# Kernel optimization log

Hardware: AMD Instinct MI355X
Metric: run time of the kernel (lower is better)

## Reference

```python
import jax, jax.numpy as jnp
import numpy as np

N = 100000
EPS = 1e-5


def sage_conv(x, edge_index, w_l, b_l, w_r):
    # PyG SAGEConv (aggr='mean'): out = lin_l(mean_{j in N(i)} x_j) + lin_r(x_i)
    src = edge_index[0]
    tgt = edge_index[1]
    msg = x[src]                                        # [E, d] gather
    agg = jax.ops.segment_sum(msg, tgt, num_segments=N)  # [N, d] scatter-add
    cnt = jax.ops.segment_sum(jnp.ones_like(tgt, dtype=x.dtype), tgt, num_segments=N)
    mean = agg / jnp.maximum(cnt, 1.0)[:, None]
    return mean @ w_l.T + b_l + x @ w_r.T


def batchnorm(h, gamma, beta):
    mu = jnp.mean(h, axis=0)
    var = jnp.var(h, axis=0)  # biased, matches torch BN training normalization
    return (h - mu) * jax.lax.rsqrt(var + EPS) * gamma + beta


def setup_inputs() -> dict:
    key = jax.random.key(0)
    ks = jax.random.split(key, 16)
    d_in, d_h, h1, h2 = 32, 64, 128, 64
    E = 1600000
    inp = {
        "x": jax.random.normal(ks[0], (N, d_in), dtype=jnp.float32),
        "edge_index": jax.random.randint(ks[1], (2, E), 0, N, dtype=jnp.int64),
        # SAGEConv 1 (bias in lin_l only)
        "w_l1": jax.random.normal(ks[2], (d_h, d_in), dtype=jnp.float32) * 0.1,
        "b_l1": jnp.zeros((d_h,), dtype=jnp.float32),
        "w_r1": jax.random.normal(ks[3], (d_h, d_in), dtype=jnp.float32) * 0.1,
        # SAGEConv 2
        "w_l2": jax.random.normal(ks[4], (d_h, d_h), dtype=jnp.float32) * 0.1,
        "b_l2": jnp.zeros((d_h,), dtype=jnp.float32),
        "w_r2": jax.random.normal(ks[5], (d_h, d_h), dtype=jnp.float32) * 0.1,
        # MLP head
        "fc1_w": jax.random.normal(ks[6], (h1, d_h), dtype=jnp.float32) * 0.1,
        "fc1_b": jnp.zeros((h1,), dtype=jnp.float32),
        "bn1_g": jnp.ones((h1,), dtype=jnp.float32),
        "bn1_b": jnp.zeros((h1,), dtype=jnp.float32),
        "fc2_w": jax.random.normal(ks[7], (h2, h1), dtype=jnp.float32) * 0.1,
        "fc2_b": jnp.zeros((h2,), dtype=jnp.float32),
        "bn2_g": jnp.ones((h2,), dtype=jnp.float32),
        "bn2_b": jnp.zeros((h2,), dtype=jnp.float32),
        "fc3_w": jax.random.normal(ks[8], (1, h2), dtype=jnp.float32) * 0.1,
        "fc3_b": jnp.zeros((1,), dtype=jnp.float32),
    }
    return inp


def reference(x, edge_index, w_l1, b_l1, w_r1, w_l2, b_l2, w_r2,
              fc1_w, fc1_b, bn1_g, bn1_b, fc2_w, fc2_b, bn2_g, bn2_b,
              fc3_w, fc3_b):
    h1 = jax.nn.relu(sage_conv(x, edge_index, w_l1, b_l1, w_r1))   # [N, 64]
    h2 = jax.nn.relu(sage_conv(h1, edge_index, w_l2, b_l2, w_r2))  # [N, 64]
    z = jax.nn.relu(batchnorm(h2 @ fc1_w.T + fc1_b, bn1_g, bn1_b))
    z = jax.nn.relu(batchnorm(z @ fc2_w.T + fc2_b, bn2_g, bn2_b))
    out = (z @ fc3_w.T + fc3_b).squeeze(-1)                        # [N]
    return (out, h1, h2)
```

## Files before the change

kernel.cpp:

```cpp
#include <hip/hip_runtime.h>

#define NN 100000
#define EPS 1e-5f

static const size_t OFF_ROWST  = 0;
static const size_t OFF_ROWEN  = 100000;
static const size_t OFF_ADJ    = 200000;
static const size_t OFF_AGG1   = 2886976;
static const size_t OFF_AGG2   = 6086976;
static const size_t OFF_PAIRS  = 2886976;
static const size_t OFF_XB     = 12486976;
static const size_t OFF_Z1     = 0;
static const size_t OFF_H1B    = 14086976;
static const size_t OFF_Z2     = 14086976;
static const size_t OFF_WSPL   = 20487000;
static const size_t OFF_BUKCNT = 20515712;
static const size_t OFF_STATS1 = 20515968;
static const size_t OFF_STATS2 = 20548736;
static const size_t OFF_COEF1  = 20565120;
static const size_t OFF_COEF2  = 20565376;
static const size_t OFF_BHIST  = 20565504;
static const size_t ZERO_START = 20515968;
static const size_t ZERO_INTS  = 49152;

#define NSLOT 128

#define WL1_HI 0
#define WL1_LO 2048
#define WR1_HI 4096
#define WR1_LO 6144
#define WL2_HI 8192
#define WL2_LO 12288
#define WR2_HI 16384
#define WR2_LO 20480
#define F1_HI  24576
#define F1_LO  32768
#define F2_HI  40960
#define F2_LO  49152

#define NBUK 256
#define BSHIFT 9
#define BCAP 10496
#define CHUNK 2048

typedef __attribute__((ext_vector_type(8))) short short8;
typedef __attribute__((ext_vector_type(4))) float f32x4;

#define MFMA_16x16x32(a, b, c) __builtin_amdgcn_mfma_f32_16x16x32_bf16(a, b, c, 0, 0, 0)

__device__ inline unsigned short f2bf(float f) {
  unsigned u = __builtin_bit_cast(unsigned, f);
  unsigned r = (u + 0x7fffu + ((u >> 16) & 1u)) >> 16;
  return (unsigned short)r;
}
__device__ inline float bf2f(unsigned short h) {
  unsigned u = ((unsigned)h) << 16;
  return __builtin_bit_cast(float, u);
}

template<bool BNIN>
__device__ inline void load_split(const float* __restrict__ p,
                                  const float* __restrict__ ca,
                                  const float* __restrict__ cc,
                                  short8& hi, short8& lo) {
  #pragma unroll
  for (int j = 0; j < 8; ++j) {
    float v = p[j];
    if (BNIN) v = fmaxf(v * ca[j] + cc[j], 0.f);
    unsigned short h = f2bf(v);
    hi[j] = (short)h;
    lo[j] = (short)f2bf(v - bf2f(h));
  }
}

struct WsplitArgs {
  const float* src[6];
  unsigned short* dhi[6];
  unsigned short* dlo[6];
  int n[6];
};
__global__ __launch_bounds__(256) void wsplit_k(WsplitArgs a) {
  int m = blockIdx.y;
  int n = a.n[m];
  for (int i = blockIdx.x * 256 + threadIdx.x; i < n; i += gridDim.x * 256) {
    float v = a.src[m][i];
    unsigned short h = f2bf(v);
    a.dhi[m][i] = h;
    a.dlo[m][i] = f2bf(v - bf2f(h));
  }
}

__global__ __launch_bounds__(256) void cvt_bf_k(const float* __restrict__ in,
                                                unsigned short* __restrict__ out,
                                                int n8) {
  int t = blockIdx.x * 256 + threadIdx.x;
  if (t >= n8) return;
  const float4* p = (const float4*)(in + (size_t)t * 8);
  float4 a = p[0], b = p[1];
  ushort4 u0, u1;
  u0.x = f2bf(a.x); u0.y = f2bf(a.y); u0.z = f2bf(a.z); u0.w = f2bf(a.w);
  u1.x = f2bf(b.x); u1.y = f2bf(b.y); u1.z = f2bf(b.z); u1.w = f2bf(b.w);
  ((ushort4*)(out + (size_t)t * 8))[0] = u0;
  ((ushort4*)(out + (size_t)t * 8))[1] = u1;
}

__global__ __launch_bounds__(256) void hista_k(const int* __restrict__ ei, int E,
                                               int* __restrict__ blockhist) {
  __shared__ int h[NBUK];
  int tid = threadIdx.x;
  h[tid] = 0;
  __syncthreads();
  int lo = blockIdx.x * CHUNK, hi = min(lo + CHUNK, E);
  for (int e = lo + tid; e < hi; e += 256) {
    int t = ei[E + e];
    if ((unsigned)t < NN) atomicAdd(&h[t >> BSHIFT], 1);
  }
  __syncthreads();
  blockhist[(size_t)blockIdx.x * NBUK + tid] = h[tid];
}

__global__ __launch_bounds__(256) void scanb_k(int* __restrict__ blockhist, int nch,
                                               int* __restrict__ bukcnt) {
  __shared__ int sh[256];
  int b = blockIdx.x, t = threadIdx.x;
  int run = 0;
  for (int base = 0; base < nch; base += 256) {
    int c = base + t;
    int v = (c < nch) ? blockhist[(size_t)c * NBUK + b] : 0;
    sh[t] = v;
    __syncthreads();
    for (int o = 1; o < 256; o <<= 1) {
      int u = (t >= o) ? sh[t - o] : 0;
      __syncthreads();
      sh[t] += u;
      __syncthreads();
    }
    if (c < nch) blockhist[(size_t)c * NBUK + b] = run + sh[t] - v;
    int tot = sh[255];
    __syncthreads();
    run += tot;
  }
  if (t == 0) bukcnt[b] = run;
}

__global__ __launch_bounds__(256) void scat_k(const int* __restrict__ ei, int E,
                                              const int* __restrict__ blockhist,
                                              unsigned* __restrict__ pairs) {
  __shared__ int wb[NBUK], cur[NBUK];
  int tid = threadIdx.x;
  wb[tid] = blockhist[(size_t)blockIdx.x * NBUK + tid];
  cur[tid] = 0;
  __syncthreads();
  int lo = blockIdx.x * CHUNK, hi = min(lo + CHUNK, E);
  for (int e = lo + tid; e < hi; e += 256) {
    int s = ei[e], t = ei[E + e];
    if ((unsigned)t >= NN) continue;
    if ((unsigned)s >= NN) s = 0;
    int b = t >> BSHIFT;
    int off = atomicAdd(&cur[b], 1);
    pairs[(size_t)b * BCAP + wb[b] + off] = ((unsigned)s << 9) | (unsigned)(t & 511);
  }
}

__global__ __launch_bounds__(256) void bfill2_k(const unsigned* __restrict__ pairs,
                                                const int* __restrict__ bukcnt,
                                                int* __restrict__ rowstart,
                                                int* __restrict__ rowend,
                                                int* __restrict__ adj) {
  __shared__ int d[512];
  __shared__ int part[256];
  int b = blockIdx.x;
  int t = threadIdx.x;
  int base = b * BCAP, cnt = bukcnt[b];
  d[t] = 0; d[t + 256] = 0;
  __syncthreads();
  for (int p = base + t; p < base + cnt; p += 256)
    atomicAdd(&d[pairs[p] & 511], 1);
  __syncthreads();
  int d0 = d[2 * t], d1 = d[2 * t + 1];
  part[t] = d0 + d1;
  __syncthreads();
  for (int o = 1; o < 256; o <<= 1) {
    int u = (t >= o) ? part[t - o] : 0;
    __syncthreads();
    part[t] += u;
    __syncthreads();
  }
  int e0 = (t > 0) ? part[t - 1] : 0;
  int e1 = e0 + d0;
  d[2 * t] = e0;
  d[2 * t + 1] = e1;
  int n0 = (b << BSHIFT) + 2 * t;
  if (n0 < NN)     { rowstart[n0]     = base + e0; rowend[n0]     = base + e1; }
  if (n0 + 1 < NN) { rowstart[n0 + 1] = base + e1; rowend[n0 + 1] = base + e1 + d1; }
  __syncthreads();
  for (int p = base + t; p < base + cnt; p += 256) {
    unsigned pr = pairs[p];
    int pos = atomicAdd(&d[pr & 511], 1);
    adj[base + pos] = (int)(pr >> 9);
  }
}

template<int K>
__global__ __launch_bounds__(256) void aggregate_bf(const unsigned short* __restrict__ xb,
                                                    const int* __restrict__ rowstart,
                                                    const int* __restrict__ rowend,
                                                    const int* __restrict__ adj,
                                                    float* __restrict__ agg) {
  constexpr int GL = K / 4;
  constexpr int NPB = 256 / GL;
  int lg = threadIdx.x & (GL - 1);
  int node = blockIdx.x * NPB + (threadIdx.x / GL);
  if (node >= NN) return;
  int s0 = rowstart[node], s1 = rowend[node];
  float4 a0 = {0,0,0,0}, a1 = {0,0,0,0}, a2 = {0,0,0,0}, a3 = {0,0,0,0};
  int e = s0;
  for (; e + 3 < s1; e += 4) {
    int i0 = adj[e], i1 = adj[e+1], i2 = adj[e+2], i3 = adj[e+3];
    ushort4 u0 = *(const ushort4*)(xb + (size_t)i0 * K + lg * 4);
    ushort4 u1 = *(const ushort4*)(xb + (size_t)i1 * K + lg * 4);
    ushort4 u2 = *(const ushort4*)(xb + (size_t)i2 * K + lg * 4);
    ushort4 u3 = *(const ushort4*)(xb + (size_t)i3 * K + lg * 4);
    a0.x += bf2f(u0.x); a0.y += bf2f(u0.y); a0.z += bf2f(u0.z); a0.w += bf2f(u0.w);
    a1.x += bf2f(u1.x); a1.y += bf2f(u1.y); a1.z += bf2f(u1.z); a1.w += bf2f(u1.w);
    a2.x += bf2f(u2.x); a2.y += bf2f(u2.y); a2.z += bf2f(u2.z); a2.w += bf2f(u2.w);
    a3.x += bf2f(u3.x); a3.y += bf2f(u3.y); a3.z += bf2f(u3.z); a3.w += bf2f(u3.w);
  }
  for (; e < s1; ++e) {
    ushort4 u = *(const ushort4*)(xb + (size_t)adj[e] * K + lg * 4);
    a0.x += bf2f(u.x); a0.y += bf2f(u.y); a0.z += bf2f(u.z); a0.w += bf2f(u.w);
  }
  float inv = 1.0f / fmaxf((float)(s1 - s0), 1.0f);
  float4 r;
  r.x = (a0.x + a1.x + a2.x + a3.x) * inv;
  r.y = (a0.y + a1.y + a2.y + a3.y) * inv;
  r.z = (a0.z + a1.z + a2.z + a3.z) * inv;
  r.w = (a0.w + a1.w + a2.w + a3.w) * inv;
  *(float4*)(agg + (size_t)node * K + lg * 4) = r;
}

template<int K, int C, bool SAGE, bool BNIN, bool RELU, bool BFOUT, bool STATS>
__global__ __launch_bounds__(256) void mfma_dense(const float* __restrict__ inA,
                                                  const float* __restrict__ inB,
                                                  const unsigned short* __restrict__ whiA,
                                                  const unsigned short* __restrict__ wloA,
                                                  const unsigned short* __restrict__ whiB,
                                                  const unsigned short* __restrict__ wloB,
                                                  const float* __restrict__ bias,
                                                  const float* __restrict__ coef,
                                                  float* __restrict__ out,
                                                  unsigned short* __restrict__ outb,
                                                  float* __restrict__ stats) {
  constexpr int KF = K / 32;
  constexpr int KC = K / 8;
  constexpr int SWZ = (KC < 8 ? KC : 8) - 1;
  __shared__ unsigned short swhiA[C * K], swloA[C * K];
  __shared__ unsigned short swhiB[SAGE ? C * K : 8], swloB[SAGE ? C * K : 8];
  __shared__ float ls[STATS ? C : 1], lq[STATS ? C : 1];

  int tid = threadIdx.x;
  for (int i = tid; i < C * KC; i += 256) {
    int col = i / KC, c = i % KC;
    int pos = col * KC + (c ^ (col & SWZ));
    ((short8*)swhiA)[pos] = ((const short8*)whiA)[i];
    ((short8*)swloA)[pos] = ((const short8*)wloA)[i];
    if (SAGE) {
      ((short8*)swhiB)[pos] = ((const short8*)whiB)[i];
      ((short8*)swloB)[pos] = ((const short8*)wloB)[i];
    }
  }
  if (STATS) {
    for (int i = tid; i < C; i += 256) { ls[i] = 0.f; lq[i] = 0.f; }
  }
  __syncthreads();

  int wid  = tid >> 6;
  int lane = tid & 63;
  int row0 = blockIdx.x * 64 + wid * 16;
  int r = lane & 15, g = lane >> 4;
  int arow = row0 + r; if (arow > NN - 1) arow = NN - 1;
  int koff = g * 8;

  short8 ahi[KF], alo[KF];
  short8 a2hi[SAGE ? KF : 1], a2lo[SAGE ? KF : 1];
  #pragma unroll
  for (int kf = 0; kf < KF; ++kf) {
    const float* p = inA + (size_t)arow * K + kf * 32 + koff;
    load_split<BNIN>(p, coef + kf * 32 + koff, coef + K + kf * 32 + koff,
                     ahi[kf], alo[kf]);
  }
  if (SAGE) {
    #pragma unroll
    for (int kf = 0; kf < KF; ++kf) {
      const float* p = inB + (size_t)arow * K + kf * 32 + koff;
      load_split<false>(p, nullptr, nullptr, a2hi[kf], a2lo[kf]);
    }
  }

  #pragma unroll
  for (int cf = 0; cf < C / 16; ++cf) {
    int col = cf * 16 + r;
    float bv = bias[col];
    f32x4 acc = {bv, bv, bv, bv};
    #pragma unroll
    for (int kf = 0; kf < KF; ++kf) {
      int c = kf * 4 + g;
      int pos = col * KC + (c ^ (col & SWZ));
      short8 whi = ((const short8*)swhiA)[pos];
      short8 wlo = ((const short8*)swloA)[pos];
      acc = MFMA_16x16x32(ahi[kf], whi, acc);
      acc = MFMA_16x16x32(ahi[kf], wlo, acc);
      acc = MFMA_16x16x32(alo[kf], whi, acc);
      if (SAGE) {
        short8 vhi = ((const short8*)swhiB)[pos];
        short8 vlo = ((const short8*)swloB)[pos];
        acc = MFMA_16x16x32(a2hi[kf], vhi, acc);
        acc = MFMA_16x16x32(a2hi[kf], vlo, acc);
        acc = MFMA_16x16x32(a2lo[kf], vhi, acc);
      }
    }
    if (STATS) {
      float s = 0.f, q = 0.f;
      #pragma unroll
      for (int j = 0; j < 4; ++j) {
        if (row0 + g * 4 + j < NN) {
          float v = acc[j];
          s += v; q += v * v;
        }
      }
      s += __shfl_xor(s, 16, 64); s += __shfl_xor(s, 32, 64);
      q += __shfl_xor(q, 16, 64); q += __shfl_xor(q, 32, 64);
      if (g == 0) { atomicAdd(&ls[col], s); atomicAdd(&lq[col], q); }
    }
    #pragma unroll
    for (int j = 0; j < 4; ++j) {
      int orow = row0 + g * 4 + j;
      if (orow < NN) {
        float v = acc[j];
        if (RELU) v = fmaxf(v, 0.f);
        out[(size_t)orow * C + col] = v;
        if (BFOUT) outb[(size_t)orow * C + col] = f2bf(v);
      }
    }
  }
  if (STATS) {
    __syncthreads();
    float* sl = stats + (size_t)(blockIdx.x & (NSLOT - 1)) * 2 * C;
    for (int i = tid; i < C; i += 256) {
      atomicAdd(&sl[i], ls[i]);
      atomicAdd(&sl[C + i], lq[i]);
    }
  }
}

__global__ void bncoef(const float* __restrict__ stats, const float* __restrict__ g,
                       const float* __restrict__ b, float* __restrict__ coef, int C) {
  int j = threadIdx.x;
  if (j >= C) return;
  float s = 0.f, q = 0.f;
  for (int sl = 0; sl < NSLOT; ++sl) {
    s += stats[(size_t)sl * 2 * C + j];
    q += stats[(size_t)sl * 2 * C + C + j];
  }
  float mu  = s * (1.0f / NN);
  float var = q * (1.0f / NN) - mu * mu;
  float a = g[j] * rsqrtf(var + EPS);
  coef[j] = a;
  coef[C + j] = b[j] - mu * a;
}

__global__ __launch_bounds__(256) void final_k(const float* __restrict__ z2,
                                               const float* __restrict__ coef,
                                               const float* __restrict__ fc3w,
                                               const float* __restrict__ fc3b,
                                               float* __restrict__ out) {
  int t = blockIdx.x * 256 + threadIdx.x;
  int i = t >> 6;
  int j = t & 63;
  if (i >= NN) return;
  float v = z2[(size_t)i * 64 + j];
  float p = fmaxf(v * coef[j] + coef[64 + j], 0.f) * fc3w[j];
  #pragma unroll
  for (int o = 32; o > 0; o >>= 1) p += __shfl_xor(p, o, 64);
  if (j == 0) out[i] = p + fc3b[0];
}

extern "C" void kernel_launch(void* const* d_in, const int* in_sizes, int n_in,
                              void* d_out, int out_size, void* d_ws, size_t ws_size,
                              hipStream_t stream) {
  const float* x     = (const float*)d_in[0];
  const int*   ei    = (const int*)d_in[1];
  const float* w_l1  = (const float*)d_in[2];
  const float* b_l1  = (const float*)d_in[3];
  const float* w_r1  = (const float*)d_in[4];
  const float* w_l2  = (const float*)d_in[5];
  const float* b_l2  = (const float*)d_in[6];
  const float* w_r2  = (const float*)d_in[7];
  const float* fc1_w = (const float*)d_in[8];
  const float* fc1_b = (const float*)d_in[9];
  const float* bn1_g = (const float*)d_in[10];
  const float* bn1_b = (const float*)d_in[11];
  const float* fc2_w = (const float*)d_in[12];
  const float* fc2_b = (const float*)d_in[13];
  const float* bn2_g = (const float*)d_in[14];
  const float* bn2_b = (const float*)d_in[15];
  const float* fc3_w = (const float*)d_in[16];
  const float* fc3_b = (const float*)d_in[17];

  const int E = in_sizes[1] / 2;

  float* ws       = (float*)d_ws;
  int*   rowstart = (int*)(ws + OFF_ROWST);
  int*   rowend   = (int*)(ws + OFF_ROWEN);
  int*   adj      = (int*)(ws + OFF_ADJ);
  float* agg1     = ws + OFF_AGG1;
  float* agg2     = ws + OFF_AGG2;
  unsigned short* xb  = (unsigned short*)(ws + OFF_XB);
  unsigned short* h1b = (unsigned short*)(ws + OFF_H1B);
  float* z1       = ws + OFF_Z1;
  float* z2       = ws + OFF_Z2;
  int*   bukcnt   = (int*)(ws + OFF_BUKCNT);
  float* stats1   = ws + OFF_STATS1;
  float* stats2   = ws + OFF_STATS2;
  float* coef1    = ws + OFF_COEF1;
  float* coef2    = ws + OFF_COEF2;
  unsigned* pairs = (unsigned*)(ws + OFF_PAIRS);
  int*   bhist    = (int*)(ws + OFF_BHIST);
  unsigned short* wspl = (unsigned short*)(ws + OFF_WSPL);

  float* outv = (float*)d_out;
  float* h1   = outv + NN;
  float* h2   = h1 + (size_t)NN * 64;

  hipMemsetAsync(ws + ZERO_START, 0, ZERO_INTS * sizeof(float), stream);

  WsplitArgs wa;
  wa.src[0] = w_l1;  wa.dhi[0] = wspl + WL1_HI; wa.dlo[0] = wspl + WL1_LO; wa.n[0] = 64 * 32;
  wa.src[1] = w_r1;  wa.dhi[1] = wspl + WR1_HI; wa.dlo[1] = wspl + WR1_LO; wa.n[1] = 64 * 32;
  wa.src[2] = w_l2;  wa.dhi[2] = wspl + WL2_HI; wa.dlo[2] = wspl + WL2_LO; wa.n[2] = 64 * 64;
  wa.src[3] = w_r2;  wa.dhi[3] = wspl + WR2_HI; wa.dlo[3] = wspl + WR2_LO; wa.n[3] = 64 * 64;
  wa.src[4] = fc1_w; wa.dhi[4] = wspl + F1_HI;  wa.dlo[4] = wspl + F1_LO;  wa.n[4] = 128 * 64;
  wa.src[5] = fc2_w; wa.dhi[5] = wspl + F2_HI;  wa.dlo[5] = wspl + F2_LO;  wa.n[5] = 64 * 128;
  wsplit_k<<<dim3(8, 6), 256, 0, stream>>>(wa);

  cvt_bf_k<<<(NN * 32 / 8 + 255) / 256, 256, 0, stream>>>(x, xb, NN * 32 / 8);

  const int NCH = (E + CHUNK - 1) / CHUNK;
  hista_k<<<NCH, 256, 0, stream>>>(ei, E, bhist);
  scanb_k<<<NBUK, 256, 0, stream>>>(bhist, NCH, bukcnt);
  scat_k<<<NCH, 256, 0, stream>>>(ei, E, bhist, pairs);
  bfill2_k<<<NBUK, 256, 0, stream>>>(pairs, bukcnt, rowstart, rowend, adj);

  const int MB = (NN + 63) / 64;

  aggregate_bf<32><<<(NN + 31) / 32, 256, 0, stream>>>(xb, rowstart, rowend, adj, agg1);
  mfma_dense<32, 64, true, false, true, true, false><<<MB, 256, 0, stream>>>(
      agg1, x, wspl + WL1_HI, wspl + WL1_LO, wspl + WR1_HI, wspl + WR1_LO,
      b_l1, nullptr, h1, h1b, nullptr);

  aggregate_bf<64><<<(NN + 15) / 16, 256, 0, stream>>>(h1b, rowstart, rowend, adj, agg2);
  mfma_dense<64, 64, true, false, true, false, false><<<MB, 256, 0, stream>>>(
      agg2, h1, wspl + WL2_HI, wspl + WL2_LO, wspl + WR2_HI, wspl + WR2_LO,
      b_l2, nullptr, h2, nullptr, nullptr);

  mfma_dense<64, 128, false, false, false, false, true><<<MB, 256, 0, stream>>>(
      h2, nullptr, wspl + F1_HI, wspl + F1_LO, nullptr, nullptr,
      fc1_b, nullptr, z1, nullptr, stats1);
  bncoef<<<1, 128, 0, stream>>>(stats1, bn1_g, bn1_b, coef1, 128);

  mfma_dense<128, 64, false, true, false, false, true><<<MB, 256, 0, stream>>>(
      z1, nullptr, wspl + F2_HI, wspl + F2_LO, nullptr, nullptr,
      fc2_b, coef1, z2, nullptr, stats2);
  bncoef<<<1, 64, 0, stream>>>(stats2, bn2_g, bn2_b, coef2, 64);

  final_k<<<(NN * 64 + 255) / 256, 256, 0, stream>>>(z2, coef2, fc3_w, fc3_b, outv);
}
```

Baseline: 241.9 us.

## Store MLP intermediates z1/z2 in bf16 and process two row tiles per block

The fc1 and fc2 pre-activations (z1, z2) are now written only as bf16 rather than fp32. fc2's input loader and the final kernel read them back as bf16, which roughly halves the bandwidth spent on these intermediates. Separately, each dense-kernel block now loops over two 64-row tiles, halving the grid and amortizing the shared-memory weight load per block. The cost is lost precision in z1/z2: BN stats are still taken from the fp32 accumulators, but normalization is then applied to bf16-rounded values.

After: 250.3 us. 1.03x slower.

```diff
diff --git a/kernel.cpp b/kernel.cpp
--- a/kernel.cpp
+++ b/kernel.cpp
@@ -10,9 +10,9 @@
 static const size_t OFF_AGG2   = 6086976;
 static const size_t OFF_PAIRS  = 2886976;
 static const size_t OFF_XB     = 12486976;
-static const size_t OFF_Z1     = 0;
+static const size_t OFF_Z1B    = 0;
 static const size_t OFF_H1B    = 14086976;
-static const size_t OFF_Z2     = 14086976;
+static const size_t OFF_Z2B    = 14086976;
 static const size_t OFF_WSPL   = 20487000;
 static const size_t OFF_BUKCNT = 20515712;
 static const size_t OFF_STATS1 = 20515968;
@@ -58,14 +58,14 @@
   return __builtin_bit_cast(float, u);
 }
 
-template<bool BNIN>
-__device__ inline void load_split(const float* __restrict__ p,
+template<bool BNIN, bool BFIN>
+__device__ inline void load_split(const void* __restrict__ p,
                                   const float* __restrict__ ca,
                                   const float* __restrict__ cc,
                                   short8& hi, short8& lo) {
   #pragma unroll
   for (int j = 0; j < 8; ++j) {
-    float v = p[j];
+    float v = BFIN ? bf2f(((const unsigned short*)p)[j]) : ((const float*)p)[j];
     if (BNIN) v = fmaxf(v * ca[j] + cc[j], 0.f);
     unsigned short h = f2bf(v);
     hi[j] = (short)h;
@@ -239,8 +239,10 @@
   *(float4*)(agg + (size_t)node * K + lg * 4) = r;
 }
 
-template<int K, int C, bool SAGE, bool BNIN, bool RELU, bool BFOUT, bool STATS>
+template<int K, int C, bool SAGE, bool BNIN, bool BFIN, bool RELU, bool FOUT,
+         bool BFOUT, bool STATS>
 __global__ __launch_bounds__(256) void mfma_dense(const float* __restrict__ inA,
+                                                  const unsigned short* __restrict__ inAb,
                                                   const float* __restrict__ inB,
                                                   const unsigned short* __restrict__ whiA,
                                                   const unsigned short* __restrict__ wloA,
@@ -276,70 +278,76 @@
 
   int wid  = tid >> 6;
   int lane = tid & 63;
-  int row0 = blockIdx.x * 64 + wid * 16;
   int r = lane & 15, g = lane >> 4;
-  int arow = row0 + r; if (arow > NN - 1) arow = NN - 1;
   int koff = g * 8;
 
-  short8 ahi[KF], alo[KF];
-  short8 a2hi[SAGE ? KF : 1], a2lo[SAGE ? KF : 1];
-  #pragma unroll
-  for (int kf = 0; kf < KF; ++kf) {
-    const float* p = inA + (size_t)arow * K + kf * 32 + koff;
-    load_split<BNIN>(p, coef + kf * 32 + koff, coef + K + kf * 32 + koff,
-                     ahi[kf], alo[kf]);
-  }
-  if (SAGE) {
+  #pragma unroll 1
+  for (int tl = 0; tl < 2; ++tl) {
+    int row0 = blockIdx.x * 128 + tl * 64 + wid * 16;
+    int arow = row0 + r; if (arow > NN - 1) arow = NN - 1;
+
+    short8 ahi[KF], alo[KF];
+    short8 a2hi[SAGE ? KF : 1], a2lo[SAGE ? KF : 1];
     #pragma unroll
     for (int kf = 0; kf < KF; ++kf) {
-      const float* p = inB + (size_t)arow * K + kf * 32 + koff;
-      load_split<false>(p, nullptr, nullptr, a2hi[kf], a2lo[kf]);
-    }
-  }
-
-  #pragma unroll
-  for (int cf = 0; cf < C / 16; ++cf) {
-    int col = cf * 16 + r;
-    float bv = bias[col];
-    f32x4 acc = {bv, bv, bv, bv};
+      const void* p = BFIN
+          ? (const void*)(inAb + (size_t)arow * K + kf * 32 + koff)
+          : (const void*)(inA  + (size_t)arow * K + kf * 32 + koff);
+      load_split<BNIN, BFIN>(p, coef + kf * 32 + koff, coef + K + kf * 32 + koff,
+                             ahi[kf], alo[kf]);
+    }
+    if (SAGE) {
+      #pragma unroll
+      for (int kf = 0; kf < KF; ++kf) {
+        const float* p = inB + (size_t)arow * K + kf * 32 + koff;
+        load_split<false, false>(p, nullptr, nullptr, a2hi[kf], a2lo[kf]);
+      }
+    }
+
     #pragma unroll
-    for (int kf = 0; kf < KF; ++kf) {
-      int c = kf * 4 + g;
-      int pos = col * KC + (c ^ (col & SWZ));
-      short8 whi = ((const short8*)swhiA)[pos];
-      short8 wlo = ((const short8*)swloA)[pos];
-      acc = MFMA_16x16x32(ahi[kf], whi, acc);
-      acc = MFMA_16x16x32(ahi[kf], wlo, acc);
-      acc = MFMA_16x16x32(alo[kf], whi, acc);
-      if (SAGE) {
-        short8 vhi = ((const short8*)swhiB)[pos];
-        short8 vlo = ((const short8*)swloB)[pos];
-        acc = MFMA_16x16x32(a2hi[kf], vhi, acc);
-        acc = MFMA_16x16x32(a2hi[kf], vlo, acc);
-        acc = MFMA_16x16x32(a2lo[kf], vhi, acc);
+    for (int cf = 0; cf < C / 16; ++cf) {
+      int col = cf * 16 + r;
+      float bv = bias[col];
+      f32x4 acc = {bv, bv, bv, bv};
+      #pragma unroll
+      for (int kf = 0; kf < KF; ++kf) {
+        int c = kf * 4 + g;
+        int pos = col * KC + (c ^ (col & SWZ));
+        short8 whi = ((const short8*)swhiA)[pos];
+        short8 wlo = ((const short8*)swloA)[pos];
+        acc = MFMA_16x16x32(ahi[kf], whi, acc);
+        acc = MFMA_16x16x32(ahi[kf], wlo, acc);
+        acc = MFMA_16x16x32(alo[kf], whi, acc);
+        if (SAGE) {
+          short8 vhi = ((const short8*)swhiB)[pos];
+          short8 vlo = ((const short8*)swloB)[pos];
+          acc = MFMA_16x16x32(a2hi[kf], vhi, acc);
+          acc = MFMA_16x16x32(a2hi[kf], vlo, acc);
+          acc = MFMA_16x16x32(a2lo[kf], vhi, acc);
+        }
       }
-    }
-    if (STATS) {
-      float s = 0.f, q = 0.f;
+      if (STATS) {
+        float s = 0.f, q = 0.f;
+        #pragma unroll
+        for (int j = 0; j < 4; ++j) {
+          if (row0 + g * 4 + j < NN) {
+            float v = acc[j];
+            s += v; q += v * v;
+          }
+        }
+        s += __shfl_xor(s, 16, 64); s += __shfl_xor(s, 32, 64);
+        q += __shfl_xor(q, 16, 64); q += __shfl_xor(q, 32, 64);
+        if (g == 0) { atomicAdd(&ls[col], s); atomicAdd(&lq[col], q); }
+      }
       #pragma unroll
       for (int j = 0; j < 4; ++j) {
-        if (row0 + g * 4 + j < NN) {
+        int orow = row0 + g * 4 + j;
+        if (orow < NN) {
           float v = acc[j];
-          s += v; q += v * v;
+          if (RELU) v = fmaxf(v, 0.f);
+          if (FOUT)  out[(size_t)orow * C + col] = v;
+          if (BFOUT) outb[(size_t)orow * C + col] = f2bf(v);
         }
-      }
-      s += __shfl_xor(s, 16, 64); s += __shfl_xor(s, 32, 64);
-      q += __shfl_xor(q, 16, 64); q += __shfl_xor(q, 32, 64);
-      if (g == 0) { atomicAdd(&ls[col], s); atomicAdd(&lq[col], q); }
-    }
-    #pragma unroll
-    for (int j = 0; j < 4; ++j) {
-      int orow = row0 + g * 4 + j;
-      if (orow < NN) {
-        float v = acc[j];
-        if (RELU) v = fmaxf(v, 0.f);
-        out[(size_t)orow * C + col] = v;
-        if (BFOUT) outb[(size_t)orow * C + col] = f2bf(v);
       }
     }
   }
@@ -369,7 +377,7 @@
   coef[C + j] = b[j] - mu * a;
 }
 
-__global__ __launch_bounds__(256) void final_k(const float* __restrict__ z2,
+__global__ __launch_bounds__(256) void final_k(const unsigned short* __restrict__ z2b,
                                                const float* __restrict__ coef,
                                                const float* __restrict__ fc3w,
                                                const float* __restrict__ fc3b,
@@ -378,7 +386,7 @@
   int i = t >> 6;
   int j = t & 63;
   if (i >= NN) return;
-  float v = z2[(size_t)i * 64 + j];
+  float v = bf2f(z2b[(size_t)i * 64 + j]);
   float p = fmaxf(v * coef[j] + coef[64 + j], 0.f) * fc3w[j];
   #pragma unroll
   for (int o = 32; o > 0; o >>= 1) p += __shfl_xor(p, o, 64);
@@ -417,8 +425,8 @@
   float* agg2     = ws + OFF_AGG2;
   unsigned short* xb  = (unsigned short*)(ws + OFF_XB);
   unsigned short* h1b = (unsigned short*)(ws + OFF_H1B);
-  float* z1       = ws + OFF_Z1;
-  float* z2       = ws + OFF_Z2;
+  unsigned short* z1b = (unsigned short*)(ws + OFF_Z1B);
+  unsigned short* z2b = (unsigned short*)(ws + OFF_Z2B);
   int*   bukcnt   = (int*)(ws + OFF_BUKCNT);
   float* stats1   = ws + OFF_STATS1;
   float* stats2   = ws + OFF_STATS2;
@@ -451,27 +459,27 @@
   scat_k<<<NCH, 256, 0, stream>>>(ei, E, bhist, pairs);
   bfill2_k<<<NBUK, 256, 0, stream>>>(pairs, bukcnt, rowstart, rowend, adj);
 
-  const int MB = (NN + 63) / 64;
+  const int MB = (NN + 127) / 128;
 
   aggregate_bf<32><<<(NN + 31) / 32, 256, 0, stream>>>(xb, rowstart, rowend, adj, agg1);
-  mfma_dense<32, 64, true, false, true, true, false><<<MB, 256, 0, stream>>>(
-      agg1, x, wspl + WL1_HI, wspl + WL1_LO, wspl + WR1_HI, wspl + WR1_LO,
+  mfma_dense<32, 64, true, false, false, true, true, true, false><<<MB, 256, 0, stream>>>(
+      agg1, nullptr, x, wspl + WL1_HI, wspl + WL1_LO, wspl + WR1_HI, wspl + WR1_LO,
       b_l1, nullptr, h1, h1b, nullptr);
 
   aggregate_bf<64><<<(NN + 15) / 16, 256, 0, stream>>>(h1b, rowstart, rowend, adj, agg2);
-  mfma_dense<64, 64, true, false, true, false, false><<<MB, 256, 0, stream>>>(
-      agg2, h1, wspl + WL2_HI, wspl + WL2_LO, wspl + WR2_HI, wspl + WR2_LO,
+  mfma_dense<64, 64, true, false, false, true, true, false, false><<<MB, 256, 0, stream>>>(
+      agg2, nullptr, h1, wspl + WL2_HI, wspl + WL2_LO, wspl + WR2_HI, wspl + WR2_LO,
       b_l2, nullptr, h2, nullptr, nullptr);
 
-  mfma_dense<64, 128, false, false, false, false, true><<<MB, 256, 0, stream>>>(
-      h2, nullptr, wspl + F1_HI, wspl + F1_LO, nullptr, nullptr,
-      fc1_b, nullptr, z1, nullptr, stats1);
+  mfma_dense<64, 128, false, false, false, false, false, true, true><<<MB, 256, 0, stream>>>(
+      h2, nullptr, nullptr, wspl + F1_HI, wspl + F1_LO, nullptr, nullptr,
+      fc1_b, nullptr, nullptr, z1b, stats1);
   bncoef<<<1, 128, 0, stream>>>(stats1, bn1_g, bn1_b, coef1, 128);
 
-  mfma_dense<128, 64, false, true, false, false, true><<<MB, 256, 0, stream>>>(
-      z1, nullptr, wspl + F2_HI, wspl + F2_LO, nullptr, nullptr,
-      fc2_b, coef1, z2, nullptr, stats2);
+  mfma_dense<128, 64, false, true, true, false, false, true, true><<<MB, 256, 0, stream>>>(
+      nullptr, z1b, nullptr, wspl + F2_HI, wspl + F2_LO, nullptr, nullptr,
+      fc2_b, coef1, nullptr, z2b, stats2);
   bncoef<<<1, 64, 0, stream>>>(stats2, bn2_g, bn2_b, coef2, 64);
 
-  final_k<<<(NN * 64 + 255) / 256, 256, 0, stream>>>(z2, coef2, fc3_w, fc3_b, outv);
-}
+  final_k<<<(NN * 64 + 255) / 256, 256, 0, stream>>>(z2b, coef2, fc3_w, fc3_b, outv);
+}
```
